# Optimization experiments

Measured on AMD Instinct MI355X. Metric: run time of the kernel, lower is better.

## Reference

```python
import jax, jax.numpy as jnp
import numpy as np
from math import comb as _comb

N, E, H, K = 20000, 320000, 128, 10
SIGMAS = jnp.asarray([100.0 ** i for i in range(10)], dtype=jnp.float32)  # all_sigmas_dist
BINOM = jnp.asarray([_comb(10, i) / 1024.0 for i in range(11)], dtype=jnp.float32)  # C(K,i)/2^K


def _lrelu(x):
    return jnp.where(x > 0, x, 0.02 * x)


def _mlp2(x, W1, b1, W2, b2):
    # Linear -> Dropout(eval=id) -> LeakyReLU(0.02) -> BatchNorm1d(eval, fresh stats = id) -> Linear
    return _lrelu(x @ W1 + b1) @ W2 + b2


def _graph_fwd(x, h, src, dst, p):
    eW1, eb1, eW2, eb2, rW1, rb1, rW2, rb2, fW1, fb1, fW2, fb2, temp = p
    xd = x[src] - x[dst]                                   # u_sub_v -> (E,3)
    d2 = jnp.sum(xd * xd, axis=1, keepdims=True)           # (E,1)
    gauss = jnp.exp(-d2 / SIGMAS)                          # (E,10) multi-sigma Gaussian
    wlap = jax.nn.relu(_mlp2(gauss, eW1, eb1, eW2, eb2))   # (E,1)
    cat = jnp.concatenate([h[src], h[dst], wlap], axis=1)  # (E,2H+1)
    r = _mlp2(cat, rW1, rb1, rW2, rb2)                     # (E,1)
    agg = jax.ops.segment_sum(r * xd, dst, num_segments=N)
    cnt = jax.ops.segment_sum(jnp.ones((src.shape[0],), x.dtype), dst, num_segments=N)
    x_new = x + agg / jnp.maximum(cnt, 1.0)[:, None]       # mean aggregation (0 for isolated)
    # --- Bern_prop (BernNet, K=10) on sym-normalized Laplacian with weights wlap ---
    w = wlap[:, 0]
    deg = jax.ops.segment_sum(w, src, num_segments=N)
    deg_safe = jnp.where(deg > 0, deg, 1.0)
    dinv = jnp.where(deg > 0, deg_safe ** -0.5, 0.0)
    norm_e = (dinv[src] * w * dinv[dst])[:, None]          # (E,1)

    def Ax(z):  # normalized adjacency matvec
        return jax.ops.segment_sum(norm_e * z[src], dst, num_segments=N)

    temp_r = jax.nn.relu(temp)
    h0 = _mlp2(h, fW1, fb1, fW2, fb2)
    tmp = [h0]
    z = h0
    for _ in range(K):
        z = z + Ax(z)            # (2I - L) z
        tmp.append(z)
    out = BINOM[0] * temp_r[0] * tmp[K]
    for i in range(K):
        z = tmp[K - i - 1]
        for _ in range(i + 1):
            z = z - Ax(z)        # L z
        out = out + BINOM[i + 1] * temp_r[i + 1] * z
    return x_new, out, temp_r


def setup_inputs() -> dict:
    ks = jax.random.split(jax.random.key(0), 12)
    s = 0.05
    return {
        "x1": jax.random.normal(ks[0], (N, 3), jnp.float32) * 5.0,
        "h1": jax.random.normal(ks[1], (N, H), jnp.float32),
        "x2": jax.random.normal(ks[2], (N, 3), jnp.float32) * 5.0,
        "h2": jax.random.normal(ks[3], (N, H), jnp.float32),
        "eW1": jax.random.normal(ks[4], (10, H), jnp.float32) * s,
        "eb1": jnp.zeros((H,), jnp.float32),
        "eW2": jax.random.normal(ks[5], (H, 1), jnp.float32) * s,
        "eb2": jnp.zeros((1,), jnp.float32),
        "rW1": jax.random.normal(ks[6], (2 * H + 1, 2 * H), jnp.float32) * s,
        "rb1": jnp.zeros((2 * H,), jnp.float32),
        "rW2": jax.random.normal(ks[7], (2 * H, 1), jnp.float32) * s,
        "rb2": jnp.zeros((1,), jnp.float32),
        "fW1": jax.random.normal(ks[8], (H, H), jnp.float32) * s,
        "fb1": jnp.zeros((H,), jnp.float32),
        "fW2": jax.random.normal(ks[9], (H, H), jnp.float32) * s,
        "fb2": jnp.zeros((H,), jnp.float32),
        "temp": jnp.ones((K + 1,), jnp.float32),
        "edge_index1": jax.random.randint(ks[10], (2, E), 0, N, jnp.int32),
        "edge_index2": jax.random.randint(ks[11], (2, E), 0, N, jnp.int32),
    }


def reference(x1, h1, x2, h2, eW1, eb1, eW2, eb2, rW1, rb1, rW2, rb2, fW1, fb1, fW2, fb2, temp, edge_index1, edge_index2):
    p = (eW1, eb1, eW2, eb2, rW1, rb1, rW2, rb2, fW1, fb1, fW2, fb2, temp)
    x1n, h1n, T1 = _graph_fwd(x1, h1, edge_index1[0], edge_index1[1], p)
    x2n, h2n, T2 = _graph_fwd(x2, h2, edge_index2[0], edge_index2[1], p)
    return (x1n, h1n, x2n, h2n, T1, T2)
```

## Files before the change

### kernel.cpp

```cpp
#include <hip/hip_runtime.h>
#include <math.h>

#define N_NODES 20000
#define N_EDGES 320000

__device__ __forceinline__ float lrelu(float x){ return x > 0.f ? x : 0.02f*x; }

__device__ __forceinline__ unsigned short f2bf(float f){
  union { float f; unsigned u; } v; v.f = f;
  unsigned r = (v.u + 0x7FFFu + ((v.u >> 16) & 1u)) >> 16;
  return (unsigned short)r;
}
__device__ __forceinline__ float bf2f(unsigned short u){
  union { unsigned u; float f; } v; v.u = ((unsigned)u) << 16; return v.f;
}

typedef __attribute__((ext_vector_type(8))) short bf16x8;
typedef __attribute__((ext_vector_type(4))) float f32x4;
typedef __attribute__((ext_vector_type(8))) unsigned short u16x8;

__global__ void k_pre(const float* __restrict__ temp, float* __restrict__ coef,
                      int* __restrict__ flags, float* __restrict__ outT1,
                      float* __restrict__ outT2,
                      const float* __restrict__ eW1, const float* __restrict__ eb1,
                      const float* __restrict__ eW2v, const float* __restrict__ rW1,
                      const float* __restrict__ rW2, const float* __restrict__ fW1,
                      const float* __restrict__ fW2,
                      float* __restrict__ wbuf,
                      unsigned short* __restrict__ WTbig,
                      unsigned short* __restrict__ WTf2,
                      int* __restrict__ counts, float* __restrict__ deg, int nZero){
  if (blockIdx.x == 0){
    if (threadIdx.x == 0){
      const double binom[11] = {1,10,45,120,210,252,210,120,45,10,1};
      double a[11]; for (int j=0;j<11;++j) a[j]=0.0;
      for (int m=0;m<=10;++m){
        double p[11]; p[0]=1.0; for (int j=1;j<11;++j) p[j]=0.0;
        for (int r2=0;r2<10-m;++r2) for (int j=10;j>=1;--j) p[j]+=p[j-1];
        for (int r2=0;r2<m;++r2)    for (int j=10;j>=1;--j) p[j]-=p[j-1];
        float t = temp[m];
        double c = (binom[m]/1024.0) * (t > 0.f ? (double)t : 0.0);
        for (int j=0;j<11;++j) a[j]+=c*p[j];
      }
      for (int j=0;j<11;++j) coef[j]=(float)a[j];
      double sIn = 0.0;
      for (int j=10;j>=0;--j){
        double sOut = sIn + fabs(a[j]);
        flags[j]    = (j==0) ? ((sIn != 0.0) ? 1 : 0) : ((sOut != 0.0) ? 1 : 0);
        flags[16+j] = (sIn  == 0.0) ? 1 : 0;
        sIn = sOut;
      }
    }
    int i = threadIdx.x;
    if (i < 11){ float t = temp[i]; t = t>0.f?t:0.f; outT1[i]=t; outT2[i]=t; }
    return;
  }
  if (blockIdx.x <= 390){
    int i = (blockIdx.x-1)*256 + threadIdx.x;
    if (i < 1280){
      float v;
      if (i < 384) v = eW1[i];
      else if (i < 512){
        int c = i-384; float s = eb1[c];
        for (int j=3;j<10;++j) s += eW1[j*128+c];
        v = s;
      } else if (i < 640) v = eW2v[i-512];
      else if (i < 960){ int k = i-640;  int l = k/20, jj = k%20;
        v = (jj<16) ? rW1[256*256 + l*16 + jj] : 0.f;
      } else            { int k = i-960; int l = k/20, jj = k%20;
        v = (jj<16) ? rW2[l*16 + jj] : 0.f;
      }
      wbuf[i] = v;
    } else if (i < 1280 + 81920){
      int j = i - 1280;
      int row = j >> 7, k = j & 127;
      float v = (row < 256) ? rW1[(size_t)k*256 + row]
              : (row < 512) ? rW1[(size_t)(128+k)*256 + (row-256)]
                            : fW1[(size_t)k*128 + (row-512)];
      WTbig[j] = f2bf(v);
    } else if (i < 1280 + 81920 + 16384){
      int j = i - 1280 - 81920; int n = j >> 7, k = j & 127;
      WTf2[j] = f2bf(fW2[(size_t)k*128 + n]);
    }
    return;
  }
  int i = (blockIdx.x-391)*256 + threadIdx.x;
  if (i < nZero){ counts[i]=0; deg[i]=0.f; }
}

__global__ void k_zero(int* counts, float* deg, int n){
  int i = blockIdx.x*blockDim.x + threadIdx.x;
  if (i < n){ counts[i]=0; deg[i]=0.f; }
}

__global__ void k_cnt_cvt(
    const int* __restrict__ dstA, const float* __restrict__ hA,
    const float* __restrict__ xA, int baseA,
    const int* __restrict__ dstB, const float* __restrict__ hB,
    const float* __restrict__ xB, int baseB,
    int splitBlocks, int* __restrict__ counts,
    unsigned short* __restrict__ h_bf, float4* __restrict__ x4){
  int b = blockIdx.x;
  const int* dst; const float* h; const float* x; int base;
  if (b < splitBlocks){ dst=dstA; h=hA; x=xA; base=baseA; }
  else { dst=dstB; h=hB; x=xB; base=baseB; b -= splitBlocks; }
  int i = b*256 + threadIdx.x;
  float4 v = reinterpret_cast<const float4*>(h)[i];
  ushort4 o;
  o.x = f2bf(v.x); o.y = f2bf(v.y); o.z = f2bf(v.z); o.w = f2bf(v.w);
  reinterpret_cast<ushort4*>(h_bf)[(size_t)base*32 + i] = o;
  if (i < N_EDGES) atomicAdd(&counts[dst[i] + base], 1);
  if (i < N_NODES) x4[base + i] = make_float4(x[3*i], x[3*i+1], x[3*i+2], 0.f);
}

__global__ void k_scanA(const int* __restrict__ counts, int* __restrict__ partial,
                        int n){
  __shared__ int ws[4];
  int tid = threadIdx.x;
  int i = blockIdx.x*256 + tid;
  int v = (i < n) ? counts[i] : 0;
  #pragma unroll
  for (int m=1;m<64;m<<=1) v += __shfl_xor(v, m);
  int lane = tid & 63, w = tid >> 6;
  if (lane==0) ws[w] = v;
  __syncthreads();
  if (tid==0) partial[blockIdx.x] = ws[0]+ws[1]+ws[2]+ws[3];
}

__global__ void k_scanB(int* __restrict__ counts, const int* __restrict__ partial,
                        int* __restrict__ rowptr, int n){
  __shared__ int ws[4];
  __shared__ int base_s;
  int tid = threadIdx.x;
  int lane = tid & 63, w = tid >> 6;
  int p = 0;
  for (int i = tid; i < (int)blockIdx.x; i += 256) p += partial[i];
  #pragma unroll
  for (int m=1;m<64;m<<=1) p += __shfl_xor(p, m);
  if (lane==0) ws[w] = p;
  __syncthreads();
  if (tid==0) base_s = ws[0]+ws[1]+ws[2]+ws[3];
  __syncthreads();
  int base = base_s;
  __syncthreads();
  int i = blockIdx.x*256 + tid;
  int v = (i < n) ? counts[i] : 0;
  int s = v;
  #pragma unroll
  for (int o2=1;o2<64;o2<<=1){
    int t2 = __shfl_up(s, o2);
    if (lane >= o2) s += t2;
  }
  if (lane==63) ws[w] = s;
  __syncthreads();
  int woff = 0;
  for (int k=0;k<w;++k) woff += ws[k];
  int incl = woff + s;
  if (i < n){
    rowptr[i] = base + incl - v;
    counts[i] = 0;
    if (i == n-1) rowptr[n] = base + incl;
  }
}

__global__ void k_fill(
    const int* __restrict__ srcA, const int* __restrict__ dstA, int baseA,
    const int* __restrict__ srcB, const int* __restrict__ dstB, int baseB,
    int splitBlocks, const int* __restrict__ rowptr, int* __restrict__ cursor,
    int* __restrict__ srcS, int* __restrict__ dstS){
  int b = blockIdx.x;
  const int* src; const int* dst; int base;
  if (b < splitBlocks){ src=srcA; dst=dstA; base=baseA; }
  else { src=srcB; dst=dstB; base=baseB; b -= splitBlocks; }
  int e = b*256 + threadIdx.x;
  if (e < N_EDGES){
    int row = dst[e] + base;
    int pos = atomicAdd(&cursor[row],1);
    int idx = rowptr[row] + pos;
    srcS[idx] = src[e] + base;
    dstS[idx] = row;
  }
}

__global__ __launch_bounds__(256) void k_gemm_mfma(
    const unsigned short* __restrict__ Abf, const unsigned short* __restrict__ WT,
    const float* __restrict__ b0, const float* __restrict__ b1, int mode, int M,
    unsigned short* __restrict__ Pb, unsigned short* __restrict__ Qb,
    unsigned short* __restrict__ Tb, unsigned short* __restrict__ h0b,
    const float* __restrict__ coefp, float* __restrict__ outH1,
    float* __restrict__ outH2, int split)
{
  __shared__ char lA[16384];
  __shared__ char lB[16384];
  int t = threadIdx.x;
  int rbase = blockIdx.x * 64;
  int cbase = blockIdx.y * 64;
  #pragma unroll
  for (int i=0;i<4;++i){
    int c = t + i*256;
    int row = c >> 4, c8 = c & 15;
    int grow = rbase + row; if (grow > M-1) grow = M-1;
    float4 av = *reinterpret_cast<const float4*>(Abf + (size_t)grow*128 + c8*8);
    *reinterpret_cast<float4*>(lA + (((row<<8) + (c8<<4)) ^ ((row&7)<<4))) = av;
    float4 wv = *reinterpret_cast<const float4*>(WT + (size_t)(cbase+row)*128 + c8*8);
    *reinterpret_cast<float4*>(lB + (((row<<8) + (c8<<4)) ^ ((row&7)<<4))) = wv;
  }
  __syncthreads();
  int l = t & 63, w = t >> 6;
  int lr = l & 15;
  int lkb = ((l >> 4) << 3) * 2;
  int sxor = (lr & 7) << 4;
  f32x4 acc[4];
  #pragma unroll
  for (int tm=0;tm<4;++tm) acc[tm] = (f32x4){0.f,0.f,0.f,0.f};
  #pragma unroll
  for (int ks=0; ks<4; ++ks){
    int kb = ks*64 + lkb;
    bf16x8 bv = *reinterpret_cast<const bf16x8*>(lB + (((((w<<4)+lr)<<8) + kb) ^ sxor));
    #pragma unroll
    for (int tm=0;tm<4;++tm){
      bf16x8 av = *reinterpret_cast<const bf16x8*>(lA + (((((tm<<4)+lr)<<8) + kb) ^ sxor));
      acc[tm] = __builtin_amdgcn_mfma_f32_16x16x32_bf16(av, bv, acc[tm], 0, 0, 0);
    }
  }
  int col = cbase + (w<<4) + lr;
  float bval;
  if (mode==0) bval = (col < 256) ? b0[col] : (col >= 512 ? b1[col-512] : 0.f);
  else         bval = b0[col];
  float c0 = (mode==1) ? coefp[0] : 0.f;
  int rsub = (l >> 4) << 2;
  #pragma unroll
  for (int tm=0;tm<4;++tm){
    #pragma unroll
    for (int r=0;r<4;++r){
      int grow = rbase + (tm<<4) + rsub + r;
      if (grow < M){
        float v = acc[tm][r];
        if (mode==0){
          if (col < 256)      Pb[(size_t)grow*256 + col]       = f2bf(v + bval);
          else if (col < 512) Qb[(size_t)grow*256 + col - 256] = f2bf(v);
          else                Tb[(size_t)grow*128 + col - 512] = f2bf(lrelu(v + bval));
        } else {
          float vb = v + bval;
          h0b[(size_t)grow*128 + col] = f2bf(vb);
          float so = c0 * vb;
          if (grow < split) outH1[(size_t)grow*128 + col] = so;
          else              outH2[(size_t)(grow-split)*128 + col] = so;
        }
      }
    }
  }
}

__global__ __launch_bounds__(256, 4) void k_edge(
    const int* __restrict__ srcS, const int* __restrict__ dstS,
    const float4* __restrict__ x4,
    const unsigned short* __restrict__ P, const unsigned short* __restrict__ Q,
    const float* __restrict__ wbuf,
    const float* __restrict__ eb2, const float* __restrict__ rb2,
    const int* __restrict__ flags,
    float* __restrict__ deg, float4* __restrict__ rxw, int nEdges)
{
  __shared__ float sw[1280];
  int tid = threadIdx.x;
  for (int i = tid; i < 1280; i += 256) sw[i] = wbuf[i];
  __syncthreads();
  int nwg = gridDim.x;
  int q = nwg >> 3, r = nwg & 7;
  int xcd = blockIdx.x & 7, idx = blockIdx.x >> 3;
  int cbase = (xcd < r) ? xcd*(q+1) : r*(q+1) + (xcd-r)*q;
  int chunk = cbase + idx;
  int l = tid & 15;
  int grp = tid >> 4;
  float base_r[8], eW2v[8];
  #pragma unroll
  for (int i=0;i<4;++i){
    float2 b = *reinterpret_cast<const float2*>(&sw[384 + 2*l + 32*i]);
    float2 w = *reinterpret_cast<const float2*>(&sw[512 + 2*l + 32*i]);
    base_r[2*i]=b.x; base_r[2*i+1]=b.y; eW2v[2*i]=w.x; eW2v[2*i+1]=w.y;
  }
  float eb2v = eb2[0], rb2v = rb2[0];
  const bool needDeg = flags[0] != 0;
  int e0 = chunk*128 + grp;
  #pragma unroll 1
  for (int k2 = 0; k2 < 8; ++k2){
    int e = e0 + (k2<<4);
    if (e >= nEdges) break;
    int s = srcS[e], d = dstS[e];
    const u16x8* Ps = reinterpret_cast<const u16x8*>(P + (size_t)s*256 + l*16);
    const u16x8* Qd = reinterpret_cast<const u16x8*>(Q + (size_t)d*256 + l*16);
    u16x8 pa = Ps[0], pb = Ps[1];
    u16x8 qa = Qd[0], qb = Qd[1];
    float4 xs = x4[s], xd = x4[d];
    float dx0 = xs.x-xd.x, dx1 = xs.y-xd.y, dx2 = xs.z-xd.z;
    float d2 = dx0*dx0 + dx1*dx1 + dx2*dx2;
    float h[8];
    #pragma unroll
    for (int i=0;i<8;++i) h[i] = base_r[i];
    const float IS[3] = {1.f,1e-2f,1e-4f};
    #pragma unroll
    for (int j=0;j<3;++j){
      float gj = __expf(-d2*IS[j]);
      #pragma unroll
      for (int i=0;i<4;++i){
        float2 w2 = *reinterpret_cast<const float2*>(&sw[j*128 + 2*l + 32*i]);
        h[2*i]   += gj*w2.x;
        h[2*i+1] += gj*w2.y;
      }
    }
    float part = 0.f;
    #pragma unroll
    for (int i=0;i<8;++i) part += lrelu(h[i])*eW2v[i];
    part += __shfl_xor(part,1); part += __shfl_xor(part,2);
    part += __shfl_xor(part,4); part += __shfl_xor(part,8);
    float wlap = part + eb2v; wlap = wlap > 0.f ? wlap : 0.f;
    float acc = 0.f;
    {
      float4 u = *reinterpret_cast<const float4*>(&sw[640 + l*20]);
      float4 w = *reinterpret_cast<const float4*>(&sw[960 + l*20]);
      acc += lrelu(bf2f((unsigned short)pa[0])+bf2f((unsigned short)qa[0])+wlap*u.x)*w.x;
      acc += lrelu(bf2f((unsigned short)pa[1])+bf2f((unsigned short)qa[1])+wlap*u.y)*w.y;
      acc += lrelu(bf2f((unsigned short)pa[2])+bf2f((unsigned short)qa[2])+wlap*u.z)*w.z;
      acc += lrelu(bf2f((unsigned short)pa[3])+bf2f((unsigned short)qa[3])+wlap*u.w)*w.w;
    }
    {
      float4 u = *reinterpret_cast<const float4*>(&sw[640 + l*20 + 4]);
      float4 w = *reinterpret_cast<const float4*>(&sw[960 + l*20 + 4]);
      acc += lrelu(bf2f((unsigned short)pa[4])+bf2f((unsigned short)qa[4])+wlap*u.x)*w.x;
      acc += lrelu(bf2f((unsigned short)pa[5])+bf2f((unsigned short)qa[5])+wlap*u.y)*w.y;
      acc += lrelu(bf2f((unsigned short)pa[6])+bf2f((unsigned short)qa[6])+wlap*u.z)*w.z;
      acc += lrelu(bf2f((unsigned short)pa[7])+bf2f((unsigned short)qa[7])+wlap*u.w)*w.w;
    }
    {
      float4 u = *reinterpret_cast<const float4*>(&sw[640 + l*20 + 8]);
      float4 w = *reinterpret_cast<const float4*>(&sw[960 + l*20 + 8]);
      acc += lrelu(bf2f((unsigned short)pb[0])+bf2f((unsigned short)qb[0])+wlap*u.x)*w.x;
      acc += lrelu(bf2f((unsigned short)pb[1])+bf2f((unsigned short)qb[1])+wlap*u.y)*w.y;
      acc += lrelu(bf2f((unsigned short)pb[2])+bf2f((unsigned short)qb[2])+wlap*u.z)*w.z;
      acc += lrelu(bf2f((unsigned short)pb[3])+bf2f((unsigned short)qb[3])+wlap*u.w)*w.w;
    }
    {
      float4 u = *reinterpret_cast<const float4*>(&sw[640 + l*20 + 12]);
      float4 w = *reinterpret_cast<const float4*>(&sw[960 + l*20 + 12]);
      acc += lrelu(bf2f((unsigned short)pb[4])+bf2f((unsigned short)qb[4])+wlap*u.x)*w.x;
      acc += lrelu(bf2f((unsigned short)pb[5])+bf2f((unsigned short)qb[5])+wlap*u.y)*w.y;
      acc += lrelu(bf2f((unsigned short)pb[6])+bf2f((unsigned short)qb[6])+wlap*u.z)*w.z;
      acc += lrelu(bf2f((unsigned short)pb[7])+bf2f((unsigned short)qb[7])+wlap*u.w)*w.w;
    }
    acc += __shfl_xor(acc,1); acc += __shfl_xor(acc,2);
    acc += __shfl_xor(acc,4); acc += __shfl_xor(acc,8);
    if (l==0){
      float r2 = acc + rb2v;
      if (needDeg) atomicAdd(&deg[s], wlap);
      rxw[e] = make_float4(r2*dx0, r2*dx1, r2*dx2, wlap);
    }
  }
}

__global__ __launch_bounds__(256) void k_post(const int* __restrict__ rowptr,
    const float4* __restrict__ rxw, const float4* __restrict__ x4,
    float* __restrict__ outX1, float* __restrict__ outX2, int split,
    const int* __restrict__ srcS, const int* __restrict__ dstS,
    const float* __restrict__ deg, const int* __restrict__ flags,
    float* __restrict__ norm, int nNodes, int aggBlocks, int nEdges)
{
  if ((int)blockIdx.x < aggBlocks){
    int lane = threadIdx.x & 63;
    int v = blockIdx.x*4 + (threadIdx.x>>6);
    if (v >= nNodes) return;
    int b = rowptr[v], e = rowptr[v+1];
    float a0=0.f,a1=0.f,a2=0.f;
    for (int i=b+lane;i<e;i+=64){ float4 f = rxw[i]; a0+=f.x; a1+=f.y; a2+=f.z; }
    #pragma unroll
    for (int m=1;m<64;m<<=1){ a0+=__shfl_xor(a0,m); a1+=__shfl_xor(a1,m); a2+=__shfl_xor(a2,m); }
    if (lane==0){
      int cnt = e-b; if (cnt < 1) cnt = 1;
      float inv = 1.0f/(float)cnt;
      float4 xv = x4[v];
      float* o = (v < split) ? (outX1 + (size_t)v*3) : (outX2 + (size_t)(v-split)*3);
      o[0] = xv.x + a0*inv;
      o[1] = xv.y + a1*inv;
      o[2] = xv.z + a2*inv;
    }
  } else {
    if (!flags[0]) return;
    int e = (blockIdx.x-aggBlocks)*256 + threadIdx.x;
    if (e < nEdges){
      float ds = deg[srcS[e]], dd = deg[dstS[e]];
      float is = ds > 0.f ? rsqrtf(ds) : 0.f;
      float id = dd > 0.f ? rsqrtf(dd) : 0.f;
      norm[e] = is * rxw[e].w * id;
    }
  }
}

__global__ __launch_bounds__(256) void k_ax(const int* __restrict__ rowptr,
    const int* __restrict__ srcS, const float* __restrict__ norm,
    const unsigned short* __restrict__ h0b,
    const float* __restrict__ coef, const int* __restrict__ flags, int j,
    float* __restrict__ zout, float* __restrict__ zin,
    float* __restrict__ outH1, float* __restrict__ outH2, int split, int nNodes)
{
  if (!flags[j]) return;
  bool scaleOnly = flags[16+j] != 0;
  bool last = (j == 0);
  float c = coef[j];
  int t = threadIdx.x & 127, sub = threadIdx.x >> 7;
  for (int v = blockIdx.x*2 + sub; v < nNodes; v += gridDim.x*2){
    float acc0 = c * bf2f(h0b[(size_t)v*128 + t]);
    if (!scaleOnly){
      int b = rowptr[v], e2 = rowptr[v+1];
      float acc1 = 0.f;
      int i = b;
      for (; i+1 < e2; i += 2){
        acc0 += norm[i]   * zin[(size_t)srcS[i]*128 + t];
        acc1 += norm[i+1] * zin[(size_t)srcS[i+1]*128 + t];
      }
      if (i < e2) acc0 += norm[i]*zin[(size_t)srcS[i]*128 + t];
      acc0 += acc1;
    }
    if (last){
      float* o = (v < split) ? (outH1 + (size_t)v*128) : (outH2 + (size_t)(v-split)*128);
      o[t] = acc0;
    } else {
      zout[(size_t)v*128 + t] = acc0;
    }
  }
}

extern "C" void kernel_launch(void* const* d_in, const int* in_sizes, int n_in,
                              void* d_out, int out_size, void* d_ws, size_t ws_size,
                              hipStream_t stream) {
  const float* x1  = (const float*)d_in[0];
  const float* h1  = (const float*)d_in[1];
  const float* x2  = (const float*)d_in[2];
  const float* h2  = (const float*)d_in[3];
  const float* eW1 = (const float*)d_in[4];
  const float* eb1 = (const float*)d_in[5];
  const float* eW2 = (const float*)d_in[6];
  const float* eb2 = (const float*)d_in[7];
  const float* rW1 = (const float*)d_in[8];
  const float* rb1 = (const float*)d_in[9];
  const float* rW2 = (const float*)d_in[10];
  const float* rb2 = (const float*)d_in[11];
  const float* fW1 = (const float*)d_in[12];
  const float* fb1 = (const float*)d_in[13];
  const float* fW2 = (const float*)d_in[14];
  const float* fb2 = (const float*)d_in[15];
  const float* temp= (const float*)d_in[16];
  const int* ei1 = (const int*)d_in[17];
  const int* ei2 = (const int*)d_in[18];

  float* out = (float*)d_out;
  float* outX1 = out;
  float* outH1 = out + 60000;
  float* outX2 = out + 2620000;
  float* outH2 = out + 2680000;
  float* outT1 = out + 5240000;
  float* outT2 = out + 5240011;

  auto needBytes = [](size_t NT, size_t ET)->size_t{
    auto al = [](size_t b){ return (b + 255) & ~(size_t)255; };
    size_t o = 0;
    o += al(NT*512);
    o += al(NT*512);
    o += al(NT*256);
    o += al(NT*256);
    o += al(NT*256);
    o += al(640*128*2);
    o += al(128*128*2);
    o += al(1280*4);
    o += al(NT*16);
    o += al(ET*4);
    o += al(ET*4);
    o += al(ET*4);
    o += al(ET*16);
    o += al(NT*4);
    o += al((NT+1)*4);
    o += al(NT*4);
    o += al(256*4);
    o += al(256) + al(256);
    return o;
  };
  const bool batched = ws_size >= needBytes(2*N_NODES, 2*N_EDGES);
  const int NT = batched ? 2*N_NODES : N_NODES;
  const int ET = batched ? 2*N_EDGES : N_EDGES;

  char* ws = (char*)d_ws;
  size_t off = 0;
  auto alloc = [&](size_t bytes)->void*{
    void* p = ws + off; off += (bytes + 255) & ~(size_t)255; return p;
  };
  unsigned short* Pb   = (unsigned short*)alloc((size_t)NT*512);
  unsigned short* Qb   = (unsigned short*)alloc((size_t)NT*512);
  unsigned short* h_bf = (unsigned short*)alloc((size_t)NT*256);
  unsigned short* t_bf = (unsigned short*)alloc((size_t)NT*256);
  unsigned short* h0b  = (unsigned short*)alloc((size_t)NT*256);
  unsigned short* WTbig= (unsigned short*)alloc((size_t)640*128*2);
  unsigned short* WTf2 = (unsigned short*)alloc((size_t)128*128*2);
  float* wbuf   = (float*)alloc((size_t)1280*4);
  float4* x4    = (float4*)alloc((size_t)NT*16);
  int*   srcS   = (int*)  alloc((size_t)ET*4);
  int*   dstS   = (int*)  alloc((size_t)ET*4);
  float* normE  = (float*)alloc((size_t)ET*4);
  float4* rxw   = (float4*)alloc((size_t)ET*16);
  int*   counts = (int*)  alloc((size_t)NT*4);
  int*   rowptr = (int*)  alloc((size_t)(NT+1)*4);
  float* deg    = (float*)alloc((size_t)NT*4);
  int*   partial= (int*)  alloc((size_t)256*4);
  float* coef   = (float*)alloc(256);
  int*   flags  = (int*)  alloc(256);

  float* z0 = (float*)h_bf;
  float* z1 = (float*)Pb;

  const int ZB = (NT + 255)/256;
  const int gemmRows = (NT + 63)/64;
  const int aggBlocks = (NT + 3)/4;
  const int normBlocks = (ET + 255)/256;
  const int scanTiles = (NT + 255)/256;
  const int edgeChunks = (ET + 127)/128;

  k_pre<<<391 + ZB, 256, 0, stream>>>(temp, coef, flags, outT1, outT2,
                                      eW1, eb1, eW2, rW1, rW2, fW1, fW2,
                                      wbuf, WTbig, WTf2, counts, deg, NT);

  if (batched){
    k_cnt_cvt<<<5000, 256, 0, stream>>>(ei1 + N_EDGES, h1, x1, 0,
                                        ei2 + N_EDGES, h2, x2, N_NODES,
                                        2500, counts, h_bf, x4);
    k_scanA<<<scanTiles, 256, 0, stream>>>(counts, partial, NT);
    k_scanB<<<scanTiles, 256, 0, stream>>>(counts, partial, rowptr, NT);
    k_fill<<<2500, 256, 0, stream>>>(ei1, ei1 + N_EDGES, 0,
                                     ei2, ei2 + N_EDGES, N_NODES,
                                     1250, rowptr, counts, srcS, dstS);

    k_gemm_mfma<<<dim3(gemmRows,10), 256, 0, stream>>>(h_bf, WTbig, rb1, fb1, 0, NT,
                                                       Pb, Qb, t_bf, nullptr,
                                                       nullptr, nullptr, nullptr, 0);
    k_gemm_mfma<<<dim3(gemmRows,2), 256, 0, stream>>>(t_bf, WTf2, fb2, nullptr, 1, NT,
                                                      nullptr, nullptr, nullptr, h0b,
                                                      coef, outH1, outH2, N_NODES);

    k_edge<<<edgeChunks, 256, 0, stream>>>(srcS, dstS, x4, Pb, Qb, wbuf, eb2, rb2,
                                           flags, deg, rxw, ET);
    k_post<<<aggBlocks + normBlocks, 256, 0, stream>>>(rowptr, rxw, x4,
                                     outX1, outX2, N_NODES, srcS, dstS, deg,
                                     flags, normE, NT, aggBlocks, ET);

    for (int j = 10; j >= 0; --j){
      float* zi = ((10-(j+1)) & 1) ? z1 : z0;
      float* zo = ((10-j) & 1) ? z1 : z0;
      if (j==10) zi = z1;
      k_ax<<<512, 256, 0, stream>>>(rowptr, srcS, normE, h0b, coef, flags, j,
                                    zo, zi, outH1, outH2, N_NODES, NT);
    }
  } else {
    for (int g = 0; g < 2; ++g){
      const float* x = g ? x2 : x1;
      const float* h = g ? h2 : h1;
      const int* src = g ? ei2 : ei1;
      const int* dst = src + N_EDGES;
      float* outX = g ? outX2 : outX1;
      float* outH = g ? outH2 : outH1;

      if (g) k_zero<<<ZB, 256, 0, stream>>>(counts, deg, NT);
      k_cnt_cvt<<<2500, 256, 0, stream>>>(dst, h, x, 0, dst, h, x, 0,
                                          2500, counts, h_bf, x4);
      k_scanA<<<scanTiles, 256, 0, stream>>>(counts, partial, NT);
      k_scanB<<<scanTiles, 256, 0, stream>>>(counts, partial, rowptr, NT);
      k_fill<<<1250, 256, 0, stream>>>(src, dst, 0, src, dst, 0,
                                       1250, rowptr, counts, srcS, dstS);

      k_gemm_mfma<<<dim3(gemmRows,10), 256, 0, stream>>>(h_bf, WTbig, rb1, fb1, 0, NT,
                                                         Pb, Qb, t_bf, nullptr,
                                                         nullptr, nullptr, nullptr, 0);
      k_gemm_mfma<<<dim3(gemmRows,2), 256, 0, stream>>>(t_bf, WTf2, fb2, nullptr, 1, NT,
                                                        nullptr, nullptr, nullptr, h0b,
                                                        coef, outH, outH, NT);

      k_edge<<<edgeChunks, 256, 0, stream>>>(srcS, dstS, x4, Pb, Qb, wbuf, eb2, rb2,
                                             flags, deg, rxw, ET);
      k_post<<<aggBlocks + normBlocks, 256, 0, stream>>>(rowptr, rxw, x4,
                                       outX, outX, NT, srcS, dstS, deg,
                                       flags, normE, NT, aggBlocks, ET);

      for (int j = 10; j >= 0; --j){
        float* zi = ((10-(j+1)) & 1) ? z1 : z0;
        float* zo = ((10-j) & 1) ? z1 : z0;
        if (j==10) zi = z1;
        k_ax<<<512, 256, 0, stream>>>(rowptr, srcS, normE, h0b, coef, flags, j,
                                      zo, zi, outH, outH, NT, NT);
      }
    }
  }
  (void)in_sizes; (void)n_in; (void)out_size; (void)ws_size;
}
```

Measured before the change: 234.4 us.

## Fuse fp32-to-bf16 conversion of node features into GEMM A-tile load

```diff
diff --git a/kernel.cpp b/kernel.cpp
--- a/kernel.cpp
+++ b/kernel.cpp
@@ -94,21 +94,14 @@
 }
 
 __global__ void k_cnt_cvt(
-    const int* __restrict__ dstA, const float* __restrict__ hA,
-    const float* __restrict__ xA, int baseA,
-    const int* __restrict__ dstB, const float* __restrict__ hB,
-    const float* __restrict__ xB, int baseB,
-    int splitBlocks, int* __restrict__ counts,
-    unsigned short* __restrict__ h_bf, float4* __restrict__ x4){
+    const int* __restrict__ dstA, const float* __restrict__ xA, int baseA,
+    const int* __restrict__ dstB, const float* __restrict__ xB, int baseB,
+    int splitBlocks, int* __restrict__ counts, float4* __restrict__ x4){
   int b = blockIdx.x;
-  const int* dst; const float* h; const float* x; int base;
-  if (b < splitBlocks){ dst=dstA; h=hA; x=xA; base=baseA; }
-  else { dst=dstB; h=hB; x=xB; base=baseB; b -= splitBlocks; }
+  const int* dst; const float* x; int base;
+  if (b < splitBlocks){ dst=dstA; x=xA; base=baseA; }
+  else { dst=dstB; x=xB; base=baseB; b -= splitBlocks; }
   int i = b*256 + threadIdx.x;
-  float4 v = reinterpret_cast<const float4*>(h)[i];
-  ushort4 o;
-  o.x = f2bf(v.x); o.y = f2bf(v.y); o.z = f2bf(v.z); o.w = f2bf(v.w);
-  reinterpret_cast<ushort4*>(h_bf)[(size_t)base*32 + i] = o;
   if (i < N_EDGES) atomicAdd(&counts[dst[i] + base], 1);
   if (i < N_NODES) x4[base + i] = make_float4(x[3*i], x[3*i+1], x[3*i+2], 0.f);
 }
@@ -183,8 +176,11 @@
 }
 
 __global__ __launch_bounds__(256) void k_gemm_mfma(
-    const unsigned short* __restrict__ Abf, const unsigned short* __restrict__ WT,
+    const float* __restrict__ A1, const float* __restrict__ A2, int splitA,
+    const unsigned short* __restrict__ Abf,
+    const unsigned short* __restrict__ WT,
     const float* __restrict__ b0, const float* __restrict__ b1, int mode, int M,
+    int nTiles, int tpb,
     unsigned short* __restrict__ Pb, unsigned short* __restrict__ Qb,
     unsigned short* __restrict__ Tb, unsigned short* __restrict__ h0b,
     const float* __restrict__ coefp, float* __restrict__ outH1,
@@ -194,58 +190,80 @@
   __shared__ char lB[16384];
   int t = threadIdx.x;
   int rbase = blockIdx.x * 64;
-  int cbase = blockIdx.y * 64;
   #pragma unroll
   for (int i=0;i<4;++i){
     int c = t + i*256;
     int row = c >> 4, c8 = c & 15;
     int grow = rbase + row; if (grow > M-1) grow = M-1;
-    float4 av = *reinterpret_cast<const float4*>(Abf + (size_t)grow*128 + c8*8);
-    *reinterpret_cast<float4*>(lA + (((row<<8) + (c8<<4)) ^ ((row&7)<<4))) = av;
-    float4 wv = *reinterpret_cast<const float4*>(WT + (size_t)(cbase+row)*128 + c8*8);
-    *reinterpret_cast<float4*>(lB + (((row<<8) + (c8<<4)) ^ ((row&7)<<4))) = wv;
-  }
-  __syncthreads();
+    int dst = ((row<<8) + (c8<<4)) ^ ((row&7)<<4);
+    if (mode == 0){
+      const float* Ar = (grow < splitA) ? (A1 + (size_t)grow*128)
+                                        : (A2 + (size_t)(grow-splitA)*128);
+      float4 f0 = *reinterpret_cast<const float4*>(Ar + c8*8);
+      float4 f1 = *reinterpret_cast<const float4*>(Ar + c8*8 + 4);
+      unsigned short u8[8];
+      u8[0]=f2bf(f0.x); u8[1]=f2bf(f0.y); u8[2]=f2bf(f0.z); u8[3]=f2bf(f0.w);
+      u8[4]=f2bf(f1.x); u8[5]=f2bf(f1.y); u8[6]=f2bf(f1.z); u8[7]=f2bf(f1.w);
+      *reinterpret_cast<float4*>(lA + dst) = *reinterpret_cast<float4*>(u8);
+    } else {
+      float4 av = *reinterpret_cast<const float4*>(Abf + (size_t)grow*128 + c8*8);
+      *reinterpret_cast<float4*>(lA + dst) = av;
+    }
+  }
   int l = t & 63, w = t >> 6;
   int lr = l & 15;
   int lkb = ((l >> 4) << 3) * 2;
   int sxor = (lr & 7) << 4;
-  f32x4 acc[4];
-  #pragma unroll
-  for (int tm=0;tm<4;++tm) acc[tm] = (f32x4){0.f,0.f,0.f,0.f};
-  #pragma unroll
-  for (int ks=0; ks<4; ++ks){
-    int kb = ks*64 + lkb;
-    bf16x8 bv = *reinterpret_cast<const bf16x8*>(lB + (((((w<<4)+lr)<<8) + kb) ^ sxor));
+  int rsub = (l >> 4) << 2;
+  for (int tt = 0; tt < tpb; ++tt){
+    int cb = blockIdx.y*tpb + tt;
+    if (cb >= nTiles) break;
+    int cbase = cb * 64;
+    __syncthreads();
+    #pragma unroll
+    for (int i=0;i<4;++i){
+      int c = t + i*256;
+      int row = c >> 4, c8 = c & 15;
+      float4 wv = *reinterpret_cast<const float4*>(WT + (size_t)(cbase+row)*128 + c8*8);
+      *reinterpret_cast<float4*>(lB + (((row<<8) + (c8<<4)) ^ ((row&7)<<4))) = wv;
+    }
+    __syncthreads();
+    f32x4 acc[4];
+    #pragma unroll
+    for (int tm=0;tm<4;++tm) acc[tm] = (f32x4){0.f,0.f,0.f,0.f};
+    #pragma unroll
+    for (int ks=0; ks<4; ++ks){
+      int kb = ks*64 + lkb;
+      bf16x8 bv = *reinterpret_cast<const bf16x8*>(lB + (((((w<<4)+lr)<<8) + kb) ^ sxor));
+      #pragma unroll
+      for (int tm=0;tm<4;++tm){
+        bf16x8 av = *reinterpret_cast<const bf16x8*>(lA + (((((tm<<4)+lr)<<8) + kb) ^ sxor));
+        acc[tm] = __builtin_amdgcn_mfma_f32_16x16x32_bf16(av, bv, acc[tm], 0, 0, 0);
+      }
+    }
+    int col = cbase + (w<<4) + lr;
+    float bval;
+    if (mode==0) bval = (col < 256) ? b0[col] : (col >= 512 ? b1[col-512] : 0.f);
+    else         bval = b0[col];
+    float c0 = (mode==1) ? coefp[0] : 0.f;
     #pragma unroll
     for (int tm=0;tm<4;++tm){
-      bf16x8 av = *reinterpret_cast<const bf16x8*>(lA + (((((tm<<4)+lr)<<8) + kb) ^ sxor));
-      acc[tm] = __builtin_amdgcn_mfma_f32_16x16x32_bf16(av, bv, acc[tm], 0, 0, 0);
-    }
-  }
-  int col = cbase + (w<<4) + lr;
-  float bval;
-  if (mode==0) bval = (col < 256) ? b0[col] : (col >= 512 ? b1[col-512] : 0.f);
-  else         bval = b0[col];
-  float c0 = (mode==1) ? coefp[0] : 0.f;
-  int rsub = (l >> 4) << 2;
-  #pragma unroll
-  for (int tm=0;tm<4;++tm){
-    #pragma unroll
-    for (int r=0;r<4;++r){
-      int grow = rbase + (tm<<4) + rsub + r;
-      if (grow < M){
-        float v = acc[tm][r];
-        if (mode==0){
-          if (col < 256)      Pb[(size_t)grow*256 + col]       = f2bf(v + bval);
-          else if (col < 512) Qb[(size_t)grow*256 + col - 256] = f2bf(v);
-          else                Tb[(size_t)grow*128 + col - 512] = f2bf(lrelu(v + bval));
-        } else {
-          float vb = v + bval;
-          h0b[(size_t)grow*128 + col] = f2bf(vb);
-          float so = c0 * vb;
-          if (grow < split) outH1[(size_t)grow*128 + col] = so;
-          else              outH2[(size_t)(grow-split)*128 + col] = so;
+      #pragma unroll
+      for (int r=0;r<4;++r){
+        int grow = rbase + (tm<<4) + rsub + r;
+        if (grow < M){
+          float v = acc[tm][r];
+          if (mode==0){
+            if (col < 256)      Pb[(size_t)grow*256 + col]       = f2bf(v + bval);
+            else if (col < 512) Qb[(size_t)grow*256 + col - 256] = f2bf(v);
+            else                Tb[(size_t)grow*128 + col - 512] = f2bf(lrelu(v + bval));
+          } else {
+            float vb = v + bval;
+            h0b[(size_t)grow*128 + col] = f2bf(vb);
+            float so = c0 * vb;
+            if (grow < split) outH1[(size_t)grow*128 + col] = so;
+            else              outH2[(size_t)(grow-split)*128 + col] = so;
+          }
         }
       }
     }
@@ -493,7 +511,7 @@
   };
   unsigned short* Pb   = (unsigned short*)alloc((size_t)NT*512);
   unsigned short* Qb   = (unsigned short*)alloc((size_t)NT*512);
-  unsigned short* h_bf = (unsigned short*)alloc((size_t)NT*256);
+  unsigned short* zpad = (unsigned short*)alloc((size_t)NT*256);
   unsigned short* t_bf = (unsigned short*)alloc((size_t)NT*256);
   unsigned short* h0b  = (unsigned short*)alloc((size_t)NT*256);
   unsigned short* WTbig= (unsigned short*)alloc((size_t)640*128*2);
@@ -511,7 +529,7 @@
   float* coef   = (float*)alloc(256);
   int*   flags  = (int*)  alloc(256);
 
-  float* z0 = (float*)h_bf;
+  float* z0 = (float*)zpad;
   float* z1 = (float*)Pb;
 
   const int ZB = (NT + 255)/256;
@@ -520,25 +538,28 @@
   const int normBlocks = (ET + 255)/256;
   const int scanTiles = (NT + 255)/256;
   const int edgeChunks = (ET + 127)/128;
+  const int cntBlocks = (N_EDGES + 255)/256;
 
   k_pre<<<391 + ZB, 256, 0, stream>>>(temp, coef, flags, outT1, outT2,
                                       eW1, eb1, eW2, rW1, rW2, fW1, fW2,
                                       wbuf, WTbig, WTf2, counts, deg, NT);
 
   if (batched){
-    k_cnt_cvt<<<5000, 256, 0, stream>>>(ei1 + N_EDGES, h1, x1, 0,
-                                        ei2 + N_EDGES, h2, x2, N_NODES,
-                                        2500, counts, h_bf, x4);
+    k_cnt_cvt<<<2*cntBlocks, 256, 0, stream>>>(ei1 + N_EDGES, x1, 0,
+                                               ei2 + N_EDGES, x2, N_NODES,
+                                               cntBlocks, counts, x4);
     k_scanA<<<scanTiles, 256, 0, stream>>>(counts, partial, NT);
     k_scanB<<<scanTiles, 256, 0, stream>>>(counts, partial, rowptr, NT);
     k_fill<<<2500, 256, 0, stream>>>(ei1, ei1 + N_EDGES, 0,
                                      ei2, ei2 + N_EDGES, N_NODES,
                                      1250, rowptr, counts, srcS, dstS);
 
-    k_gemm_mfma<<<dim3(gemmRows,10), 256, 0, stream>>>(h_bf, WTbig, rb1, fb1, 0, NT,
-                                                       Pb, Qb, t_bf, nullptr,
-                                                       nullptr, nullptr, nullptr, 0);
-    k_gemm_mfma<<<dim3(gemmRows,2), 256, 0, stream>>>(t_bf, WTf2, fb2, nullptr, 1, NT,
+    k_gemm_mfma<<<dim3(gemmRows,2), 256, 0, stream>>>(h1, h2, N_NODES, nullptr,
+                                                      WTbig, rb1, fb1, 0, NT, 10, 5,
+                                                      Pb, Qb, t_bf, nullptr,
+                                                      nullptr, nullptr, nullptr, 0);
+    k_gemm_mfma<<<dim3(gemmRows,1), 256, 0, stream>>>(nullptr, nullptr, 0, t_bf,
+                                                      WTf2, fb2, nullptr, 1, NT, 2, 2,
                                                       nullptr, nullptr, nullptr, h0b,
                                                       coef, outH1, outH2, N_NODES);
 
@@ -565,17 +586,19 @@
       float* outH = g ? outH2 : outH1;
 
       if (g) k_zero<<<ZB, 256, 0, stream>>>(counts, deg, NT);
-      k_cnt_cvt<<<2500, 256, 0, stream>>>(dst, h, x, 0, dst, h, x, 0,
-                                          2500, counts, h_bf, x4);
+      k_cnt_cvt<<<cntBlocks, 256, 0, stream>>>(dst, x, 0, dst, x, 0,
+                                               cntBlocks, counts, x4);
       k_scanA<<<scanTiles, 256, 0, stream>>>(counts, partial, NT);
       k_scanB<<<scanTiles, 256, 0, stream>>>(counts, partial, rowptr, NT);
       k_fill<<<1250, 256, 0, stream>>>(src, dst, 0, src, dst, 0,
                                        1250, rowptr, counts, srcS, dstS);
 
-      k_gemm_mfma<<<dim3(gemmRows,10), 256, 0, stream>>>(h_bf, WTbig, rb1, fb1, 0, NT,
-                                                         Pb, Qb, t_bf, nullptr,
-                                                         nullptr, nullptr, nullptr, 0);
-      k_gemm_mfma<<<dim3(gemmRows,2), 256, 0, stream>>>(t_bf, WTf2, fb2, nullptr, 1, NT,
+      k_gemm_mfma<<<dim3(gemmRows,2), 256, 0, stream>>>(h, h, NT, nullptr,
+                                                        WTbig, rb1, fb1, 0, NT, 10, 5,
+                                                        Pb, Qb, t_bf, nullptr,
+                                                        nullptr, nullptr, nullptr, 0);
+      k_gemm_mfma<<<dim3(gemmRows,1), 256, 0, stream>>>(nullptr, nullptr, 0, t_bf,
+                                                        WTf2, fb2, nullptr, 1, NT, 2, 2,
                                                         nullptr, nullptr, nullptr, h0b,
                                                         coef, outH, outH, NT);
 
```

New measurement: 260.0 us. +10.9%, slower.
